# Kernel optimization log

Measured on AMD Instinct MI355X. Metric: run time of the kernel, lower is better.

Reference implementation:

```python
import jax, jax.numpy as jnp
import numpy as np

B, N, E = 2, 20000, 160000
D, U = 1, 100          # input_dim, num_units
IN = D + U             # 101
NEG_SLOPE = 0.2        # PyG GATv2Conv default


def setup_inputs() -> dict:
    key = jax.random.key(0)
    ks = jax.random.split(key, 20)
    s = 0.1
    inp = {
        "inputs": jax.random.normal(ks[0], (B, N * D), jnp.float32),
        "state": jax.random.normal(ks[1], (B, N * U), jnp.float32),
        "src": jax.random.randint(ks[2], (E,), 0, N),
        "dst": jax.random.randint(ks[3], (E,), 0, N),
        # GATv2Conv(101, 200) params: lin_l, lin_r, att, out-bias
        "Wl1": jax.random.normal(ks[4], (IN, 2 * U), jnp.float32) * s,
        "bl1": jax.random.normal(ks[5], (2 * U,), jnp.float32) * s,
        "Wr1": jax.random.normal(ks[6], (IN, 2 * U), jnp.float32) * s,
        "br1": jax.random.normal(ks[7], (2 * U,), jnp.float32) * s,
        "att1": jax.random.normal(ks[8], (2 * U,), jnp.float32) * s,
        "bg1": jax.random.normal(ks[9], (2 * U,), jnp.float32) * s,
        "bias0": jax.random.normal(ks[10], (2 * U,), jnp.float32) * s,
        # GATv2Conv(101, 100) params
        "Wl2": jax.random.normal(ks[11], (IN, U), jnp.float32) * s,
        "bl2": jax.random.normal(ks[12], (U,), jnp.float32) * s,
        "Wr2": jax.random.normal(ks[13], (IN, U), jnp.float32) * s,
        "br2": jax.random.normal(ks[14], (U,), jnp.float32) * s,
        "att2": jax.random.normal(ks[15], (U,), jnp.float32) * s,
        "bg2": jax.random.normal(ks[16], (U,), jnp.float32) * s,
        "bias1": jax.random.normal(ks[17], (U,), jnp.float32) * s,
    }
    return inp


def _gatv2(x, src_f, dst_f, Wl, bl, Wr, br, att, bg):
    # x: (B, N, IN); edges (with self-loops) flow src -> dst.
    xl = x @ Wl + bl                                   # (B, N, C) source transform
    xr = x @ Wr + br                                   # (B, N, C) target transform
    msg = jax.nn.leaky_relu(xl[:, src_f] + xr[:, dst_f], NEG_SLOPE)  # (B, Ef, C)
    e = jnp.einsum('bec,c->be', msg, att)              # (B, Ef) attention logits
    seg_max = jax.vmap(lambda v: jax.ops.segment_max(v, dst_f, num_segments=N))(e)
    ea = jnp.exp(e - seg_max[:, dst_f])
    denom = jax.vmap(lambda v: jax.ops.segment_sum(v, dst_f, num_segments=N))(ea)
    alpha = ea / denom[:, dst_f]                       # per-target softmax
    out = jax.vmap(
        lambda a, xs: jax.ops.segment_sum(a[:, None] * xs, dst_f, num_segments=N)
    )(alpha, xl[:, src_f])                             # (B, N, C)
    return out + bg


def reference(inputs, state, src, dst,
              Wl1, bl1, Wr1, br1, att1, bg1, bias0,
              Wl2, bl2, Wr2, br2, att2, bg2, bias1):
    loops = jnp.arange(N)
    src_f = jnp.concatenate([src, loops])              # PyG adds self-loops
    dst_f = jnp.concatenate([dst, loops])
    inputs3 = inputs.reshape(B, N, D)
    state3 = state.reshape(B, N, U)

    # _gc1: GATv2(101 -> 200) + bias_0, sigmoid gates r, u
    xs = jnp.concatenate([inputs3, state3], axis=2)    # (B, N, 101)
    g1 = _gatv2(xs, src_f, dst_f, Wl1, bl1, Wr1, br1, att1, bg1) + bias0
    val = jax.nn.sigmoid(g1)                           # (B, N, 200)
    r = val[..., :U].reshape(B, N * U)
    u = val[..., U:].reshape(B, N * U)

    # _gc2: GATv2(101 -> 100) on [inputs, r*state] + bias_1, tanh
    xs2 = jnp.concatenate([inputs3, (r * state).reshape(B, N, U)], axis=2)
    c = jnp.tanh(_gatv2(xs2, src_f, dst_f, Wl2, bl2, Wr2, br2, att2, bg2) + bias1)
    c = c.reshape(B, N * U)

    new_state = u * state + (1.0 - u) * c              # (B, N*U)
    return new_state
```

## Files before the change

kernel.cpp:

```cpp
#include <hip/hip_runtime.h>
#include <stdint.h>

typedef __attribute__((ext_vector_type(8))) short short8;
typedef __attribute__((ext_vector_type(4))) short short4v;
typedef __attribute__((ext_vector_type(4))) float f32x4;

static constexpr int BB = 2, NN = 20000, UU = 100;
static constexpr int MT = BB * NN;
static constexpr int MPAD = 40192;
static constexpr float NEG = 0.2f;

__device__ __forceinline__ float b2f(short s) {
  union { uint32_t u; float f; } cv; cv.u = ((uint32_t)(uint16_t)s) << 16; return cv.f;
}
__device__ __forceinline__ short f2b(float x) {
  union { float f; uint32_t u; } cv; cv.f = x;
  uint32_t r = cv.u + 0x7FFFu + ((cv.u >> 16) & 1u);
  return (short)(r >> 16);
}

template<int CTRL>
__device__ __forceinline__ float dppadd(float x) {
  int v = __builtin_amdgcn_update_dpp(0, __float_as_int(x), CTRL, 0xF, 0xF, false);
  return x + __int_as_float(v);
}
__device__ __forceinline__ float red32(float x) {
  x = dppadd<0x121>(x);
  x = dppadd<0x122>(x);
  x = dppadd<0x124>(x);
  x = dppadd<0x128>(x);
  return x + __shfl_xor(x, 16);
}


__global__ void k_prep(const float* __restrict__ inp, const float* __restrict__ st,
                       const float* __restrict__ Wl1, const float* __restrict__ Wr1,
                       const float* __restrict__ Wl2, const float* __restrict__ Wr2,
                       short* __restrict__ A, short* __restrict__ BT1,
                       short* __restrict__ BT2, int* __restrict__ cursor) {
  int t = blockIdx.x * 256 + threadIdx.x;
  if (t < MT * 16) {
    int r = t >> 4, g = t & 15;
    short8 v;
#pragma unroll
    for (int j = 0; j < 8; ++j) {
      int e = g * 8 + j;
      float x = 0.f;
      if (e == 0) x = inp[r];
      else if (e <= 100) x = st[(size_t)r * 100 + e - 1];
      v[j] = f2b(x);
    }
    *(short8*)(A + (size_t)r * 128 + (g << 3)) = v;
  }
  if (t < 512 * 16) {
    int n = t >> 4, g = t & 15;
    short8 v;
#pragma unroll
    for (int j = 0; j < 8; ++j) {
      int k = g * 8 + j;
      float x = 0.f;
      if (k < 101 && n < 400)
        x = (n < 200) ? Wl1[(size_t)k * 200 + n] : Wr1[(size_t)k * 200 + n - 200];
      v[j] = f2b(x);
    }
    *(short8*)(BT1 + (size_t)n * 128 + (g << 3)) = v;
  }
  if (t < 256 * 16) {
    int n = t >> 4, g = t & 15;
    short8 v;
#pragma unroll
    for (int j = 0; j < 8; ++j) {
      int k = g * 8 + j;
      int ksrc = (k < 100) ? k + 1 : ((k == 100) ? 0 : -1);
      float x = 0.f;
      if (ksrc >= 0 && n < 200)
        x = (n < 100) ? Wl2[(size_t)ksrc * 100 + n] : Wr2[(size_t)ksrc * 100 + n - 100];
      v[j] = f2b(x);
    }
    *(short8*)(BT2 + (size_t)n * 128 + (g << 3)) = v;
  }
  if (t < NN) cursor[t] = 0;
}


__global__ void k_hist(const int* __restrict__ dst, int E, int* __restrict__ hist) {
  int e = blockIdx.x * 256 + threadIdx.x;
  if (e < E) atomicAdd(&hist[dst[e]], 1);
}

__global__ __launch_bounds__(1024) void k_scan(int* __restrict__ histcur,
                                               int* __restrict__ rowptr, int N, int E) {
  __shared__ int part[1024];
  int t = threadIdx.x;
  int CH = (N + 1023) / 1024;
  int beg = t * CH; if (beg > N) beg = N;
  int end = beg + CH; if (end > N) end = N;
  int s = 0;
  for (int i = beg; i < end; ++i) s += histcur[i];
  part[t] = s;
  __syncthreads();
  for (int off = 1; off < 1024; off <<= 1) {
    int v = (t >= off) ? part[t - off] : 0;
    __syncthreads();
    part[t] += v;
    __syncthreads();
  }
  int base = (t == 0) ? 0 : part[t - 1];
  for (int i = beg; i < end; ++i) {
    int h = histcur[i];
    rowptr[i] = base;
    histcur[i] = base;
    base += h;
  }
  if (t == 1023) rowptr[N] = part[1023];
}

__global__ void k_scatter(const int* __restrict__ src, const int* __restrict__ dst, int E,
                          int* __restrict__ cursor, int* __restrict__ col) {
  int e = blockIdx.x * 256 + threadIdx.x;
  if (e < E) {
    int p = atomicAdd(&cursor[dst[e]], 1);
    col[p] = src[e];
  }
}


template<int NOUT, int SPLIT, int NTW>
__global__ __launch_bounds__(256) void k_gemmd(
    const short* __restrict__ A, const short* __restrict__ BT,
    const float* __restrict__ bias_l, const float* __restrict__ bias_r,
    short* __restrict__ X) {
  int w = threadIdx.x >> 6, lane = threadIdx.x & 63;
  int m0 = (blockIdx.x * 4 + w) * 64;
  int lrow = lane & 15, lk = lane >> 4;

  short8 a[4][4];
#pragma unroll
  for (int kk = 0; kk < 4; ++kk)
#pragma unroll
    for (int j = 0; j < 4; ++j)
      a[kk][j] = *(const short8*)(A + ((size_t)m0 + j * 16 + lrow) * 128 + lk * 8 + kk * 32);

#pragma unroll
  for (int nt = 0; nt < NTW; ++nt) {
    int nbase = (blockIdx.y * NTW + nt) * 64;
    f32x4 acc[4][4];
#pragma unroll
    for (int i = 0; i < 4; ++i)
#pragma unroll
      for (int j = 0; j < 4; ++j) acc[i][j] = (f32x4){0.f, 0.f, 0.f, 0.f};

#pragma unroll
    for (int kk = 0; kk < 4; ++kk) {
      short8 b[4];
#pragma unroll
      for (int i = 0; i < 4; ++i)
        b[i] = *(const short8*)(BT + ((size_t)nbase + i * 16 + lrow) * 128 + lk * 8 + kk * 32);
#pragma unroll
      for (int i = 0; i < 4; ++i)
#pragma unroll
        for (int j = 0; j < 4; ++j)
          acc[i][j] = __builtin_amdgcn_mfma_f32_16x16x32_bf16(b[i], a[kk][j], acc[i][j], 0, 0, 0);
    }

#pragma unroll
    for (int i = 0; i < 4; ++i) {
      int ch = nbase + i * 16 + lk * 4;
      if (ch < NOUT) {
        f32x4 bv = (ch < SPLIT) ? *(const f32x4*)(bias_l + ch)
                                : *(const f32x4*)(bias_r + (ch - SPLIT));
        int cbase = (ch < SPLIT) ? ch : 2 * SPLIT + (ch - SPLIT);
#pragma unroll
        for (int j = 0; j < 4; ++j) {
          int m = m0 + j * 16 + lrow;
          if (m < MT) {
            int b_   = (m >= NN) ? 1 : 0;
            int node = m - b_ * NN;
            short4v wv;
#pragma unroll
            for (int r = 0; r < 4; ++r) wv[r] = f2b(acc[i][j][r] + bv[r]);
            *(short4v*)(X + (size_t)node * (4 * SPLIT) + cbase + b_ * SPLIT) = wv;
          }
        }
      }
    }
  }
}


#define EDGE1(S, NUM, DEN, NCH, STRIDE)                                            \
  { short8 v_ = *(const short8*)(xb + (size_t)(S) * STRIDE);                       \
    float e_ = 0.f;                                                                \
    _Pragma("unroll") for (int q = 0; q < NCH; ++q) {                              \
      float x_ = b2f(v_[q]); float m_ = x_ + xrv[q];                               \
      m_ = (m_ > 0.f) ? m_ : NEG * m_; e_ = fmaf(m_, attv[q], e_); }               \
    e_ = red32(e_);                                                                \
    float p_ = __expf(e_); DEN += p_;                                              \
    _Pragma("unroll") for (int q = 0; q < NCH; ++q)                                \
      NUM[q] = fmaf(p_, b2f(v_[q]), NUM[q]); }

__global__ __launch_bounds__(256) void k_agg1(
    const short* __restrict__ X1, const int* __restrict__ rowptr, const int* __restrict__ col,
    const float* __restrict__ att, const float* __restrict__ bgv, const float* __restrict__ bias0,
    const float* __restrict__ st, const float* __restrict__ inp,
    short* __restrict__ A2, float* __restrict__ uu) {
  int w = threadIdx.x >> 6, lane = threadIdx.x & 63;
  int n = blockIdx.x * 4 + w;
  if (n >= NN) return;
  int half = lane >> 5, ll = lane & 31;
  int c0 = (ll < 25 ? ll : 24) * 8;
  int idx = half * NN + n;
  const short* xb = X1 + (size_t)half * 200 + c0;

  float attv[8], xrv[8], num[8];
  {
    f32x4 a0 = (f32x4){0,0,0,0}, a1 = (f32x4){0,0,0,0};
    if (ll < 25) { a0 = *(const f32x4*)(att + c0); a1 = *(const f32x4*)(att + c0 + 4); }
#pragma unroll
    for (int q = 0; q < 4; ++q) { attv[q] = a0[q]; attv[4 + q] = a1[q]; }
    short8 xr8 = *(const short8*)(X1 + (size_t)n * 800 + 400 + half * 200 + c0);
#pragma unroll
    for (int q = 0; q < 8; ++q) xrv[q] = (ll < 25) ? b2f(xr8[q]) : 0.f;
  }
  float denom;
  {
    short8 v = *(const short8*)(xb + (size_t)n * 800);
    float xs[8], e = 0.f;
#pragma unroll
    for (int q = 0; q < 8; ++q) {
      xs[q] = b2f(v[q]);
      float msg = xs[q] + xrv[q];
      msg = (msg > 0.f) ? msg : NEG * msg;
      e = fmaf(msg, attv[q], e);
    }
    e = red32(e);
    float pe = __expf(e);
    denom = pe;
#pragma unroll
    for (int q = 0; q < 8; ++q) num[q] = pe * xs[q];
  }

  int beg = rowptr[n], end = rowptr[n + 1];
  int deg = end - beg;
  int degc = min(deg, 64);
  int cv = 0;
  if (deg > 0) cv = col[beg + (lane < degc ? lane : 0)];
  int p = 0;
  for (; p + 2 <= degc; p += 2) {
    int s0 = __shfl(cv, p), s1 = __shfl(cv, p + 1);
    short8 v0 = *(const short8*)(xb + (size_t)s0 * 800);
    short8 v1 = *(const short8*)(xb + (size_t)s1 * 800);
    float e0 = 0.f, e1 = 0.f;
#pragma unroll
    for (int q = 0; q < 8; ++q) {
      float x, m_;
      x = b2f(v0[q]); m_ = x + xrv[q]; m_ = (m_ > 0.f) ? m_ : NEG * m_; e0 = fmaf(m_, attv[q], e0);
      x = b2f(v1[q]); m_ = x + xrv[q]; m_ = (m_ > 0.f) ? m_ : NEG * m_; e1 = fmaf(m_, attv[q], e1);
    }
    e0 = red32(e0); e1 = red32(e1);
    float pe0 = __expf(e0), pe1 = __expf(e1);
    denom += pe0 + pe1;
#pragma unroll
    for (int q = 0; q < 8; ++q)
      num[q] = fmaf(pe1, b2f(v1[q]), fmaf(pe0, b2f(v0[q]), num[q]));
  }
  if (p < degc) {
    int s0 = __shfl(cv, p);
    EDGE1(s0, num, denom, 8, 800);
  }
  for (int t = 64; t < deg; ++t) { int s = col[beg + t]; EDGE1(s, num, denom, 8, 800); }

  float invd = 1.f / denom;
  if (ll < 25) {
    f32x4 g0 = *(const f32x4*)(bgv + c0),   g1 = *(const f32x4*)(bgv + c0 + 4);
    f32x4 h0 = *(const f32x4*)(bias0 + c0), h1 = *(const f32x4*)(bias0 + c0 + 4);
    float vq[8];
#pragma unroll
    for (int q = 0; q < 4; ++q) {
      float o0 = fmaf(num[q], invd, g0[q] + h0[q]);
      vq[q] = 1.f / (1.f + __expf(-o0));
      float o1 = fmaf(num[4 + q], invd, g1[q] + h1[q]);
      vq[4 + q] = 1.f / (1.f + __expf(-o1));
    }
    size_t sb = (size_t)idx * UU;
    if (ll < 12) {
      f32x4 s0 = *(const f32x4*)(st + sb + c0), s1 = *(const f32x4*)(st + sb + c0 + 4);
      short8 wv;
#pragma unroll
      for (int q = 0; q < 4; ++q) { wv[q] = f2b(vq[q] * s0[q]); wv[4 + q] = f2b(vq[4 + q] * s1[q]); }
      *(short8*)(A2 + (size_t)idx * 128 + (ll << 3)) = wv;
    } else if (ll == 12) {
      f32x4 s0 = *(const f32x4*)(st + sb + 96);
      short8 wv;
#pragma unroll
      for (int q = 0; q < 4; ++q) wv[q] = f2b(vq[q] * s0[q]);
      wv[4] = f2b(inp[idx]); wv[5] = 0; wv[6] = 0; wv[7] = 0;
      *(short8*)(A2 + (size_t)idx * 128 + (12 << 3)) = wv;
      *(f32x4*)(uu + sb) = (f32x4){vq[4], vq[5], vq[6], vq[7]};
    } else {
      int uo = c0 - 100;
      *(f32x4*)(uu + sb + uo)     = (f32x4){vq[0], vq[1], vq[2], vq[3]};
      *(f32x4*)(uu + sb + uo + 4) = (f32x4){vq[4], vq[5], vq[6], vq[7]};
      if (ll < 16) {
        short8 z = (short8){0,0,0,0,0,0,0,0};
        *(short8*)(A2 + (size_t)idx * 128 + (ll << 3)) = z;
      }
    }
  }
}

__global__ __launch_bounds__(256) void k_agg2(
    const short* __restrict__ X2, const int* __restrict__ rowptr, const int* __restrict__ col,
    const float* __restrict__ att, const float* __restrict__ bgv, const float* __restrict__ bias1,
    const float* __restrict__ st, float* __restrict__ out) {
  int w = threadIdx.x >> 6, lane = threadIdx.x & 63;
  int n = blockIdx.x * 4 + w;
  if (n >= NN) return;
  int half = lane >> 5, ll = lane & 31;
  int c0 = (ll < 25 ? ll : 24) * 4;
  int idx = half * NN + n;
  const short* xb = X2 + (size_t)half * 100 + c0;

  float attv[4], xrv[4], num[4];
  {
    f32x4 a0 = (f32x4){0,0,0,0};
    if (ll < 25) a0 = *(const f32x4*)(att + c0);
#pragma unroll
    for (int q = 0; q < 4; ++q) attv[q] = a0[q];
    short4v xr4 = *(const short4v*)(X2 + (size_t)n * 400 + 200 + half * 100 + c0);
#pragma unroll
    for (int q = 0; q < 4; ++q) xrv[q] = (ll < 25) ? b2f(xr4[q]) : 0.f;
  }
  float denom;
  {
    short4v v = *(const short4v*)(xb + (size_t)n * 400);
    float xs[4], e = 0.f;
#pragma unroll
    for (int q = 0; q < 4; ++q) {
      xs[q] = b2f(v[q]);
      float msg = xs[q] + xrv[q];
      msg = (msg > 0.f) ? msg : NEG * msg;
      e = fmaf(msg, attv[q], e);
    }
    e = red32(e);
    float pe = __expf(e);
    denom = pe;
#pragma unroll
    for (int q = 0; q < 4; ++q) num[q] = pe * xs[q];
  }

  int beg = rowptr[n], end = rowptr[n + 1];
  int deg = end - beg;
  int degc = min(deg, 64);
  int cv = 0;
  if (deg > 0) cv = col[beg + (lane < degc ? lane : 0)];
  int p = 0;
  for (; p + 2 <= degc; p += 2) {
    int s0 = __shfl(cv, p), s1 = __shfl(cv, p + 1);
    short4v v0 = *(const short4v*)(xb + (size_t)s0 * 400);
    short4v v1 = *(const short4v*)(xb + (size_t)s1 * 400);
    float e0 = 0.f, e1 = 0.f;
#pragma unroll
    for (int q = 0; q < 4; ++q) {
      float x, m_;
      x = b2f(v0[q]); m_ = x + xrv[q]; m_ = (m_ > 0.f) ? m_ : NEG * m_; e0 = fmaf(m_, attv[q], e0);
      x = b2f(v1[q]); m_ = x + xrv[q]; m_ = (m_ > 0.f) ? m_ : NEG * m_; e1 = fmaf(m_, attv[q], e1);
    }
    e0 = red32(e0); e1 = red32(e1);
    float pe0 = __expf(e0), pe1 = __expf(e1);
    denom += pe0 + pe1;
#pragma unroll
    for (int q = 0; q < 4; ++q)
      num[q] = fmaf(pe1, b2f(v1[q]), fmaf(pe0, b2f(v0[q]), num[q]));
  }
  if (p < degc) {
    int s0 = __shfl(cv, p);
    { short4v v_ = *(const short4v*)(xb + (size_t)s0 * 400);
      float e_ = 0.f;
#pragma unroll
      for (int q = 0; q < 4; ++q) {
        float x_ = b2f(v_[q]); float m_ = x_ + xrv[q];
        m_ = (m_ > 0.f) ? m_ : NEG * m_; e_ = fmaf(m_, attv[q], e_);
      }
      e_ = red32(e_);
      float p_ = __expf(e_); denom += p_;
#pragma unroll
      for (int q = 0; q < 4; ++q) num[q] = fmaf(p_, b2f(v_[q]), num[q]);
    }
  }
  for (int t = 64; t < deg; ++t) {
    int s = col[beg + t];
    { short4v v_ = *(const short4v*)(xb + (size_t)s * 400);
      float e_ = 0.f;
#pragma unroll
      for (int q = 0; q < 4; ++q) {
        float x_ = b2f(v_[q]); float m_ = x_ + xrv[q];
        m_ = (m_ > 0.f) ? m_ : NEG * m_; e_ = fmaf(m_, attv[q], e_);
      }
      e_ = red32(e_);
      float p_ = __expf(e_); denom += p_;
#pragma unroll
      for (int q = 0; q < 4; ++q) num[q] = fmaf(p_, b2f(v_[q]), num[q]);
    }
  }

  float invd = 1.f / denom;
  if (ll < 25) {
    f32x4 g0 = *(const f32x4*)(bgv + c0);
    f32x4 h0 = *(const f32x4*)(bias1 + c0);
    size_t sb = (size_t)idx * UU;
    f32x4 uv = *(const f32x4*)(out + sb + c0);
    f32x4 sv = *(const f32x4*)(st + sb + c0);
    f32x4 res;
#pragma unroll
    for (int q = 0; q < 4; ++q) {
      float o   = fmaf(num[q], invd, g0[q] + h0[q]);
      float cvh = tanhf(o);
      res[q] = uv[q] * sv[q] + (1.f - uv[q]) * cvh;
    }
    *(f32x4*)(out + sb + c0) = res;
  }
}


extern "C" void kernel_launch(void* const* d_in, const int* in_sizes, int n_in,
                              void* d_out, int out_size, void* d_ws, size_t ws_size,
                              hipStream_t stream) {
  const float* inp  = (const float*)d_in[0];
  const float* st   = (const float*)d_in[1];
  const int*   src  = (const int*)d_in[2];
  const int*   dst  = (const int*)d_in[3];
  const float* Wl1  = (const float*)d_in[4];
  const float* bl1  = (const float*)d_in[5];
  const float* Wr1  = (const float*)d_in[6];
  const float* br1  = (const float*)d_in[7];
  const float* att1 = (const float*)d_in[8];
  const float* bg1  = (const float*)d_in[9];
  const float* bias0= (const float*)d_in[10];
  const float* Wl2  = (const float*)d_in[11];
  const float* bl2  = (const float*)d_in[12];
  const float* Wr2  = (const float*)d_in[13];
  const float* br2  = (const float*)d_in[14];
  const float* att2 = (const float*)d_in[15];
  const float* bg2  = (const float*)d_in[16];
  const float* bias1= (const float*)d_in[17];

  const int N = NN;
  const int E = in_sizes[2];

  short* X1  = (short*)d_ws;
  short* X2  = X1;
  short* Aws = X1 + (size_t)NN * 800;
  short* BT1 = Aws + (size_t)MPAD * 128;
  short* BT2 = BT1 + 512 * 128;
  int* rowptr = (int*)(BT2 + 256 * 128);
  int* cursor = rowptr + (N + 1);
  int* col    = cursor + N;

  k_prep<<<(MT * 16 + 255) / 256, 256, 0, stream>>>(inp, st, Wl1, Wr1, Wl2, Wr2,
                                                    Aws, BT1, BT2, cursor);
  k_hist<<<(E + 255) / 256, 256, 0, stream>>>(dst, E, cursor);
  k_scan<<<1, 1024, 0, stream>>>(cursor, rowptr, N, E);
  k_scatter<<<(E + 255) / 256, 256, 0, stream>>>(src, dst, E, cursor, col);
  {
    dim3 g(157, 4);
    k_gemmd<400, 200, 2><<<g, 256, 0, stream>>>(Aws, BT1, bl1, br1, X1);
  }
  k_agg1<<<(NN + 3) / 4, 256, 0, stream>>>(X1, rowptr, col, att1, bg1, bias0, st, inp,
                                           Aws, (float*)d_out);
  {
    dim3 g(157, 2);
    k_gemmd<200, 100, 2><<<g, 256, 0, stream>>>(Aws, BT2, bl2, br2, X2);
  }
  k_agg2<<<(NN + 3) / 4, 256, 0, stream>>>(X2, rowptr, col, att2, bg2, bias1, st,
                                           (float*)d_out);
}
```

Baseline: 178.9 us.

## Fuse edge histogram into first GEMM launch and make aggregation kernels persistent

The edge-degree histogram is folded into the first GEMM launch as extra trailing blocks, so one kernel launch disappears and the atomics can overlap with the MFMA work. The GEMM grid is flattened to 1D and decodes its tile coordinates from blockIdx. Both aggregation kernels become grid-stride persistent kernels with 1024 blocks, loading the per-channel att/bias vectors once per warp instead of once per node. The cost is a fixed grid size that may balance load worse, plus modulo index arithmetic in the GEMM.

```diff
diff --git a/kernel.cpp b/kernel.cpp
--- a/kernel.cpp
+++ b/kernel.cpp
@@ -82,11 +82,6 @@
   if (t < NN) cursor[t] = 0;
 }
 
-
-__global__ void k_hist(const int* __restrict__ dst, int E, int* __restrict__ hist) {
-  int e = blockIdx.x * 256 + threadIdx.x;
-  if (e < E) atomicAdd(&hist[dst[e]], 1);
-}
 
 __global__ __launch_bounds__(1024) void k_scan(int* __restrict__ histcur,
                                                int* __restrict__ rowptr, int N, int E) {
@@ -129,9 +124,17 @@
 __global__ __launch_bounds__(256) void k_gemmd(
     const short* __restrict__ A, const short* __restrict__ BT,
     const float* __restrict__ bias_l, const float* __restrict__ bias_r,
-    short* __restrict__ X) {
-  int w = threadIdx.x >> 6, lane = threadIdx.x & 63;
-  int m0 = (blockIdx.x * 4 + w) * 64;
+    short* __restrict__ X, int nbg,
+    const int* __restrict__ dstE, int E, int* __restrict__ hist) {
+  int tid = threadIdx.x;
+  if ((int)blockIdx.x >= nbg) {
+    int e = (blockIdx.x - nbg) * 256 + tid;
+    if (e < E) atomicAdd(&hist[dstE[e]], 1);
+    return;
+  }
+  int bx = blockIdx.x % 157, by = blockIdx.x / 157;
+  int w = tid >> 6, lane = tid & 63;
+  int m0 = (bx * 4 + w) * 64;
   int lrow = lane & 15, lk = lane >> 4;
 
   short8 a[4][4];
@@ -143,7 +146,7 @@
 
 #pragma unroll
   for (int nt = 0; nt < NTW; ++nt) {
-    int nbase = (blockIdx.y * NTW + nt) * 64;
+    int nbase = (by * NTW + nt) * 64;
     f32x4 acc[4][4];
 #pragma unroll
     for (int i = 0; i < 4; ++i)
@@ -204,106 +207,116 @@
     const float* __restrict__ att, const float* __restrict__ bgv, const float* __restrict__ bias0,
     const float* __restrict__ st, const float* __restrict__ inp,
     short* __restrict__ A2, float* __restrict__ uu) {
-  int w = threadIdx.x >> 6, lane = threadIdx.x & 63;
-  int n = blockIdx.x * 4 + w;
-  if (n >= NN) return;
+  int lane = threadIdx.x & 63;
+  int gw = blockIdx.x * 4 + (threadIdx.x >> 6);
+  int NW = gridDim.x * 4;
   int half = lane >> 5, ll = lane & 31;
   int c0 = (ll < 25 ? ll : 24) * 8;
-  int idx = half * NN + n;
   const short* xb = X1 + (size_t)half * 200 + c0;
 
-  float attv[8], xrv[8], num[8];
+  float attv[8];
+  f32x4 g0 = (f32x4){0,0,0,0}, g1 = (f32x4){0,0,0,0};
+  f32x4 h0 = (f32x4){0,0,0,0}, h1 = (f32x4){0,0,0,0};
   {
     f32x4 a0 = (f32x4){0,0,0,0}, a1 = (f32x4){0,0,0,0};
-    if (ll < 25) { a0 = *(const f32x4*)(att + c0); a1 = *(const f32x4*)(att + c0 + 4); }
+    if (ll < 25) {
+      a0 = *(const f32x4*)(att + c0);   a1 = *(const f32x4*)(att + c0 + 4);
+      g0 = *(const f32x4*)(bgv + c0);   g1 = *(const f32x4*)(bgv + c0 + 4);
+      h0 = *(const f32x4*)(bias0 + c0); h1 = *(const f32x4*)(bias0 + c0 + 4);
+    }
 #pragma unroll
     for (int q = 0; q < 4; ++q) { attv[q] = a0[q]; attv[4 + q] = a1[q]; }
-    short8 xr8 = *(const short8*)(X1 + (size_t)n * 800 + 400 + half * 200 + c0);
-#pragma unroll
-    for (int q = 0; q < 8; ++q) xrv[q] = (ll < 25) ? b2f(xr8[q]) : 0.f;
-  }
-  float denom;
-  {
-    short8 v = *(const short8*)(xb + (size_t)n * 800);
-    float xs[8], e = 0.f;
-#pragma unroll
-    for (int q = 0; q < 8; ++q) {
-      xs[q] = b2f(v[q]);
-      float msg = xs[q] + xrv[q];
-      msg = (msg > 0.f) ? msg : NEG * msg;
-      e = fmaf(msg, attv[q], e);
-    }
-    e = red32(e);
-    float pe = __expf(e);
-    denom = pe;
-#pragma unroll
-    for (int q = 0; q < 8; ++q) num[q] = pe * xs[q];
-  }
-
-  int beg = rowptr[n], end = rowptr[n + 1];
-  int deg = end - beg;
-  int degc = min(deg, 64);
-  int cv = 0;
-  if (deg > 0) cv = col[beg + (lane < degc ? lane : 0)];
-  int p = 0;
-  for (; p + 2 <= degc; p += 2) {
-    int s0 = __shfl(cv, p), s1 = __shfl(cv, p + 1);
-    short8 v0 = *(const short8*)(xb + (size_t)s0 * 800);
-    short8 v1 = *(const short8*)(xb + (size_t)s1 * 800);
-    float e0 = 0.f, e1 = 0.f;
-#pragma unroll
-    for (int q = 0; q < 8; ++q) {
-      float x, m_;
-      x = b2f(v0[q]); m_ = x + xrv[q]; m_ = (m_ > 0.f) ? m_ : NEG * m_; e0 = fmaf(m_, attv[q], e0);
-      x = b2f(v1[q]); m_ = x + xrv[q]; m_ = (m_ > 0.f) ? m_ : NEG * m_; e1 = fmaf(m_, attv[q], e1);
-    }
-    e0 = red32(e0); e1 = red32(e1);
-    float pe0 = __expf(e0), pe1 = __expf(e1);
-    denom += pe0 + pe1;
-#pragma unroll
-    for (int q = 0; q < 8; ++q)
-      num[q] = fmaf(pe1, b2f(v1[q]), fmaf(pe0, b2f(v0[q]), num[q]));
-  }
-  if (p < degc) {
-    int s0 = __shfl(cv, p);
-    EDGE1(s0, num, denom, 8, 800);
-  }
-  for (int t = 64; t < deg; ++t) { int s = col[beg + t]; EDGE1(s, num, denom, 8, 800); }
-
-  float invd = 1.f / denom;
-  if (ll < 25) {
-    f32x4 g0 = *(const f32x4*)(bgv + c0),   g1 = *(const f32x4*)(bgv + c0 + 4);
-    f32x4 h0 = *(const f32x4*)(bias0 + c0), h1 = *(const f32x4*)(bias0 + c0 + 4);
-    float vq[8];
-#pragma unroll
-    for (int q = 0; q < 4; ++q) {
-      float o0 = fmaf(num[q], invd, g0[q] + h0[q]);
-      vq[q] = 1.f / (1.f + __expf(-o0));
-      float o1 = fmaf(num[4 + q], invd, g1[q] + h1[q]);
-      vq[4 + q] = 1.f / (1.f + __expf(-o1));
-    }
-    size_t sb = (size_t)idx * UU;
-    if (ll < 12) {
-      f32x4 s0 = *(const f32x4*)(st + sb + c0), s1 = *(const f32x4*)(st + sb + c0 + 4);
-      short8 wv;
-#pragma unroll
-      for (int q = 0; q < 4; ++q) { wv[q] = f2b(vq[q] * s0[q]); wv[4 + q] = f2b(vq[4 + q] * s1[q]); }
-      *(short8*)(A2 + (size_t)idx * 128 + (ll << 3)) = wv;
-    } else if (ll == 12) {
-      f32x4 s0 = *(const f32x4*)(st + sb + 96);
-      short8 wv;
-#pragma unroll
-      for (int q = 0; q < 4; ++q) wv[q] = f2b(vq[q] * s0[q]);
-      wv[4] = f2b(inp[idx]); wv[5] = 0; wv[6] = 0; wv[7] = 0;
-      *(short8*)(A2 + (size_t)idx * 128 + (12 << 3)) = wv;
-      *(f32x4*)(uu + sb) = (f32x4){vq[4], vq[5], vq[6], vq[7]};
-    } else {
-      int uo = c0 - 100;
-      *(f32x4*)(uu + sb + uo)     = (f32x4){vq[0], vq[1], vq[2], vq[3]};
-      *(f32x4*)(uu + sb + uo + 4) = (f32x4){vq[4], vq[5], vq[6], vq[7]};
-      if (ll < 16) {
-        short8 z = (short8){0,0,0,0,0,0,0,0};
-        *(short8*)(A2 + (size_t)idx * 128 + (ll << 3)) = z;
+  }
+
+  for (int n = gw; n < NN; n += NW) {
+    int idx = half * NN + n;
+    float xrv[8], num[8];
+    {
+      short8 xr8 = *(const short8*)(X1 + (size_t)n * 800 + 400 + half * 200 + c0);
+#pragma unroll
+      for (int q = 0; q < 8; ++q) xrv[q] = (ll < 25) ? b2f(xr8[q]) : 0.f;
+    }
+    float denom;
+    {
+      short8 v = *(const short8*)(xb + (size_t)n * 800);
+      float xs[8], e = 0.f;
+#pragma unroll
+      for (int q = 0; q < 8; ++q) {
+        xs[q] = b2f(v[q]);
+        float msg = xs[q] + xrv[q];
+        msg = (msg > 0.f) ? msg : NEG * msg;
+        e = fmaf(msg, attv[q], e);
+      }
+      e = red32(e);
+      float pe = __expf(e);
+      denom = pe;
+#pragma unroll
+      for (int q = 0; q < 8; ++q) num[q] = pe * xs[q];
+    }
+
+    int beg = rowptr[n], end = rowptr[n + 1];
+    int deg = end - beg;
+    int degc = min(deg, 64);
+    int cv = 0;
+    if (deg > 0) cv = col[beg + (lane < degc ? lane : 0)];
+    int p = 0;
+    for (; p + 2 <= degc; p += 2) {
+      int s0 = __shfl(cv, p), s1 = __shfl(cv, p + 1);
+      short8 v0 = *(const short8*)(xb + (size_t)s0 * 800);
+      short8 v1 = *(const short8*)(xb + (size_t)s1 * 800);
+      float e0 = 0.f, e1 = 0.f;
+#pragma unroll
+      for (int q = 0; q < 8; ++q) {
+        float x, m_;
+        x = b2f(v0[q]); m_ = x + xrv[q]; m_ = (m_ > 0.f) ? m_ : NEG * m_; e0 = fmaf(m_, attv[q], e0);
+        x = b2f(v1[q]); m_ = x + xrv[q]; m_ = (m_ > 0.f) ? m_ : NEG * m_; e1 = fmaf(m_, attv[q], e1);
+      }
+      e0 = red32(e0); e1 = red32(e1);
+      float pe0 = __expf(e0), pe1 = __expf(e1);
+      denom += pe0 + pe1;
+#pragma unroll
+      for (int q = 0; q < 8; ++q)
+        num[q] = fmaf(pe1, b2f(v1[q]), fmaf(pe0, b2f(v0[q]), num[q]));
+    }
+    if (p < degc) {
+      int s0 = __shfl(cv, p);
+      EDGE1(s0, num, denom, 8, 800);
+    }
+    for (int t = 64; t < deg; ++t) { int s = col[beg + t]; EDGE1(s, num, denom, 8, 800); }
+
+    float invd = 1.f / denom;
+    if (ll < 25) {
+      float vq[8];
+#pragma unroll
+      for (int q = 0; q < 4; ++q) {
+        float o0 = fmaf(num[q], invd, g0[q] + h0[q]);
+        vq[q] = 1.f / (1.f + __expf(-o0));
+        float o1 = fmaf(num[4 + q], invd, g1[q] + h1[q]);
+        vq[4 + q] = 1.f / (1.f + __expf(-o1));
+      }
+      size_t sb = (size_t)idx * UU;
+      if (ll < 12) {
+        f32x4 s0 = *(const f32x4*)(st + sb + c0), s1 = *(const f32x4*)(st + sb + c0 + 4);
+        short8 wv;
+#pragma unroll
+        for (int q = 0; q < 4; ++q) { wv[q] = f2b(vq[q] * s0[q]); wv[4 + q] = f2b(vq[4 + q] * s1[q]); }
+        *(short8*)(A2 + (size_t)idx * 128 + (ll << 3)) = wv;
+      } else if (ll == 12) {
+        f32x4 s0 = *(const f32x4*)(st + sb + 96);
+        short8 wv;
+#pragma unroll
+        for (int q = 0; q < 4; ++q) wv[q] = f2b(vq[q] * s0[q]);
+        wv[4] = f2b(inp[idx]); wv[5] = 0; wv[6] = 0; wv[7] = 0;
+        *(short8*)(A2 + (size_t)idx * 128 + (12 << 3)) = wv;
+        *(f32x4*)(uu + sb) = (f32x4){vq[4], vq[5], vq[6], vq[7]};
+      } else {
+        int uo = c0 - 100;
+        *(f32x4*)(uu + sb + uo)     = (f32x4){vq[0], vq[1], vq[2], vq[3]};
+        *(f32x4*)(uu + sb + uo + 4) = (f32x4){vq[4], vq[5], vq[6], vq[7]};
+        if (ll < 16) {
+          short8 z = (short8){0,0,0,0,0,0,0,0};
+          *(short8*)(A2 + (size_t)idx * 128 + (ll << 3)) = z;
+        }
       }
     }
   }
@@ -313,112 +326,121 @@
     const short* __restrict__ X2, const int* __restrict__ rowptr, const int* __restrict__ col,
     const float* __restrict__ att, const float* __restrict__ bgv, const float* __restrict__ bias1,
     const float* __restrict__ st, float* __restrict__ out) {
-  int w = threadIdx.x >> 6, lane = threadIdx.x & 63;
-  int n = blockIdx.x * 4 + w;
-  if (n >= NN) return;
+  int lane = threadIdx.x & 63;
+  int gw = blockIdx.x * 4 + (threadIdx.x >> 6);
+  int NW = gridDim.x * 4;
   int half = lane >> 5, ll = lane & 31;
   int c0 = (ll < 25 ? ll : 24) * 4;
-  int idx = half * NN + n;
   const short* xb = X2 + (size_t)half * 100 + c0;
 
-  float attv[4], xrv[4], num[4];
+  float attv[4];
+  f32x4 g0 = (f32x4){0,0,0,0}, h0 = (f32x4){0,0,0,0};
   {
     f32x4 a0 = (f32x4){0,0,0,0};
-    if (ll < 25) a0 = *(const f32x4*)(att + c0);
+    if (ll < 25) {
+      a0 = *(const f32x4*)(att + c0);
+      g0 = *(const f32x4*)(bgv + c0);
+      h0 = *(const f32x4*)(bias1 + c0);
+    }
 #pragma unroll
     for (int q = 0; q < 4; ++q) attv[q] = a0[q];
-    short4v xr4 = *(const short4v*)(X2 + (size_t)n * 400 + 200 + half * 100 + c0);
-#pragma unroll
-    for (int q = 0; q < 4; ++q) xrv[q] = (ll < 25) ? b2f(xr4[q]) : 0.f;
-  }
-  float denom;
-  {
-    short4v v = *(const short4v*)(xb + (size_t)n * 400);
-    float xs[4], e = 0.f;
-#pragma unroll
-    for (int q = 0; q < 4; ++q) {
-      xs[q] = b2f(v[q]);
-      float msg = xs[q] + xrv[q];
-      msg = (msg > 0.f) ? msg : NEG * msg;
-      e = fmaf(msg, attv[q], e);
-    }
-    e = red32(e);
-    float pe = __expf(e);
-    denom = pe;
-#pragma unroll
-    for (int q = 0; q < 4; ++q) num[q] = pe * xs[q];
-  }
-
-  int beg = rowptr[n], end = rowptr[n + 1];
-  int deg = end - beg;
-  int degc = min(deg, 64);
-  int cv = 0;
-  if (deg > 0) cv = col[beg + (lane < degc ? lane : 0)];
-  int p = 0;
-  for (; p + 2 <= degc; p += 2) {
-    int s0 = __shfl(cv, p), s1 = __shfl(cv, p + 1);
-    short4v v0 = *(const short4v*)(xb + (size_t)s0 * 400);
-    short4v v1 = *(const short4v*)(xb + (size_t)s1 * 400);
-    float e0 = 0.f, e1 = 0.f;
-#pragma unroll
-    for (int q = 0; q < 4; ++q) {
-      float x, m_;
-      x = b2f(v0[q]); m_ = x + xrv[q]; m_ = (m_ > 0.f) ? m_ : NEG * m_; e0 = fmaf(m_, attv[q], e0);
-      x = b2f(v1[q]); m_ = x + xrv[q]; m_ = (m_ > 0.f) ? m_ : NEG * m_; e1 = fmaf(m_, attv[q], e1);
-    }
-    e0 = red32(e0); e1 = red32(e1);
-    float pe0 = __expf(e0), pe1 = __expf(e1);
-    denom += pe0 + pe1;
-#pragma unroll
-    for (int q = 0; q < 4; ++q)
-      num[q] = fmaf(pe1, b2f(v1[q]), fmaf(pe0, b2f(v0[q]), num[q]));
-  }
-  if (p < degc) {
-    int s0 = __shfl(cv, p);
-    { short4v v_ = *(const short4v*)(xb + (size_t)s0 * 400);
-      float e_ = 0.f;
+  }
+
+  for (int n = gw; n < NN; n += NW) {
+    int idx = half * NN + n;
+    float xrv[4], num[4];
+    {
+      short4v xr4 = *(const short4v*)(X2 + (size_t)n * 400 + 200 + half * 100 + c0);
+#pragma unroll
+      for (int q = 0; q < 4; ++q) xrv[q] = (ll < 25) ? b2f(xr4[q]) : 0.f;
+    }
+    float denom;
+    {
+      short4v v = *(const short4v*)(xb + (size_t)n * 400);
+      float xs[4], e = 0.f;
 #pragma unroll
       for (int q = 0; q < 4; ++q) {
-        float x_ = b2f(v_[q]); float m_ = x_ + xrv[q];
-        m_ = (m_ > 0.f) ? m_ : NEG * m_; e_ = fmaf(m_, attv[q], e_);
-      }
-      e_ = red32(e_);
-      float p_ = __expf(e_); denom += p_;
-#pragma unroll
-      for (int q = 0; q < 4; ++q) num[q] = fmaf(p_, b2f(v_[q]), num[q]);
-    }
-  }
-  for (int t = 64; t < deg; ++t) {
-    int s = col[beg + t];
-    { short4v v_ = *(const short4v*)(xb + (size_t)s * 400);
-      float e_ = 0.f;
+        xs[q] = b2f(v[q]);
+        float msg = xs[q] + xrv[q];
+        msg = (msg > 0.f) ? msg : NEG * msg;
+        e = fmaf(msg, attv[q], e);
+      }
+      e = red32(e);
+      float pe = __expf(e);
+      denom = pe;
+#pragma unroll
+      for (int q = 0; q < 4; ++q) num[q] = pe * xs[q];
+    }
+
+    int beg = rowptr[n], end = rowptr[n + 1];
+    int deg = end - beg;
+    int degc = min(deg, 64);
+    int cv = 0;
+    if (deg > 0) cv = col[beg + (lane < degc ? lane : 0)];
+    int p = 0;
+    for (; p + 2 <= degc; p += 2) {
+      int s0 = __shfl(cv, p), s1 = __shfl(cv, p + 1);
+      short4v v0 = *(const short4v*)(xb + (size_t)s0 * 400);
+      short4v v1 = *(const short4v*)(xb + (size_t)s1 * 400);
+      float e0 = 0.f, e1 = 0.f;
 #pragma unroll
       for (int q = 0; q < 4; ++q) {
-        float x_ = b2f(v_[q]); float m_ = x_ + xrv[q];
-        m_ = (m_ > 0.f) ? m_ : NEG * m_; e_ = fmaf(m_, attv[q], e_);
-      }
-      e_ = red32(e_);
-      float p_ = __expf(e_); denom += p_;
-#pragma unroll
-      for (int q = 0; q < 4; ++q) num[q] = fmaf(p_, b2f(v_[q]), num[q]);
-    }
-  }
-
-  float invd = 1.f / denom;
-  if (ll < 25) {
-    f32x4 g0 = *(const f32x4*)(bgv + c0);
-    f32x4 h0 = *(const f32x4*)(bias1 + c0);
-    size_t sb = (size_t)idx * UU;
-    f32x4 uv = *(const f32x4*)(out + sb + c0);
-    f32x4 sv = *(const f32x4*)(st + sb + c0);
-    f32x4 res;
-#pragma unroll
-    for (int q = 0; q < 4; ++q) {
-      float o   = fmaf(num[q], invd, g0[q] + h0[q]);
-      float cvh = tanhf(o);
-      res[q] = uv[q] * sv[q] + (1.f - uv[q]) * cvh;
-    }
-    *(f32x4*)(out + sb + c0) = res;
+        float x, m_;
+        x = b2f(v0[q]); m_ = x + xrv[q]; m_ = (m_ > 0.f) ? m_ : NEG * m_; e0 = fmaf(m_, attv[q], e0);
+        x = b2f(v1[q]); m_ = x + xrv[q]; m_ = (m_ > 0.f) ? m_ : NEG * m_; e1 = fmaf(m_, attv[q], e1);
+      }
+      e0 = red32(e0); e1 = red32(e1);
+      float pe0 = __expf(e0), pe1 = __expf(e1);
+      denom += pe0 + pe1;
+#pragma unroll
+      for (int q = 0; q < 4; ++q)
+        num[q] = fmaf(pe1, b2f(v1[q]), fmaf(pe0, b2f(v0[q]), num[q]));
+    }
+    if (p < degc) {
+      int s0 = __shfl(cv, p);
+      { short4v v_ = *(const short4v*)(xb + (size_t)s0 * 400);
+        float e_ = 0.f;
+#pragma unroll
+        for (int q = 0; q < 4; ++q) {
+          float x_ = b2f(v_[q]); float m_ = x_ + xrv[q];
+          m_ = (m_ > 0.f) ? m_ : NEG * m_; e_ = fmaf(m_, attv[q], e_);
+        }
+        e_ = red32(e_);
+        float p_ = __expf(e_); denom += p_;
+#pragma unroll
+        for (int q = 0; q < 4; ++q) num[q] = fmaf(p_, b2f(v_[q]), num[q]);
+      }
+    }
+    for (int t = 64; t < deg; ++t) {
+      int s = col[beg + t];
+      { short4v v_ = *(const short4v*)(xb + (size_t)s * 400);
+        float e_ = 0.f;
+#pragma unroll
+        for (int q = 0; q < 4; ++q) {
+          float x_ = b2f(v_[q]); float m_ = x_ + xrv[q];
+          m_ = (m_ > 0.f) ? m_ : NEG * m_; e_ = fmaf(m_, attv[q], e_);
+        }
+        e_ = red32(e_);
+        float p_ = __expf(e_); denom += p_;
+#pragma unroll
+        for (int q = 0; q < 4; ++q) num[q] = fmaf(p_, b2f(v_[q]), num[q]);
+      }
+    }
+
+    float invd = 1.f / denom;
+    if (ll < 25) {
+      size_t sb = (size_t)idx * UU;
+      f32x4 uv = *(const f32x4*)(out + sb + c0);
+      f32x4 sv = *(const f32x4*)(st + sb + c0);
+      f32x4 res;
+#pragma unroll
+      for (int q = 0; q < 4; ++q) {
+        float o   = fmaf(num[q], invd, g0[q] + h0[q]);
+        float cvh = tanhf(o);
+        res[q] = uv[q] * sv[q] + (1.f - uv[q]) * cvh;
+      }
+      *(f32x4*)(out + sb + c0) = res;
+    }
   }
 }
 
@@ -459,19 +481,18 @@
 
   k_prep<<<(MT * 16 + 255) / 256, 256, 0, stream>>>(inp, st, Wl1, Wr1, Wl2, Wr2,
                                                     Aws, BT1, BT2, cursor);
-  k_hist<<<(E + 255) / 256, 256, 0, stream>>>(dst, E, cursor);
+  {
+    int nbg = 157 * 4;
+    int nbh = (E + 255) / 256;
+    k_gemmd<400, 200, 2><<<nbg + nbh, 256, 0, stream>>>(Aws, BT1, bl1, br1, X1,
+                                                        nbg, dst, E, cursor);
+  }
   k_scan<<<1, 1024, 0, stream>>>(cursor, rowptr, N, E);
   k_scatter<<<(E + 255) / 256, 256, 0, stream>>>(src, dst, E, cursor, col);
-  {
-    dim3 g(157, 4);
-    k_gemmd<400, 200, 2><<<g, 256, 0, stream>>>(Aws, BT1, bl1, br1, X1);
-  }
-  k_agg1<<<(NN + 3) / 4, 256, 0, stream>>>(X1, rowptr, col, att1, bg1, bias0, st, inp,
-                                           Aws, (float*)d_out);
-  {
-    dim3 g(157, 2);
-    k_gemmd<200, 100, 2><<<g, 256, 0, stream>>>(Aws, BT2, bl2, br2, X2);
-  }
-  k_agg2<<<(NN + 3) / 4, 256, 0, stream>>>(X2, rowptr, col, att2, bg2, bias1, st,
-                                           (float*)d_out);
-}
+  k_agg1<<<1024, 256, 0, stream>>>(X1, rowptr, col, att1, bg1, bias0, st, inp,
+                                   Aws, (float*)d_out);
+  k_gemmd<200, 100, 2><<<157 * 2, 256, 0, stream>>>(Aws, BT2, bl2, br2, X2,
+                                                    157 * 2, nullptr, 0, nullptr);
+  k_agg2<<<1024, 256, 0, stream>>>(X2, rowptr, col, att2, bg2, bias1, st,
+                                   (float*)d_out);
+}
```

Measured after the change: 182.8 us. +2.2%, slower.
